# Performance work log

Measured on AMD Instinct MI355X. Metric: run time of the kernel, lower is better.

Reference implementation:

```python
import jax, jax.numpy as jnp
import numpy as np

DIM = 768
HEADS = 12
HEAD_DIM = DIM // HEADS
HIDDEN = 4 * DIM
LS_INIT = 1e-5
EPS = 1e-5


def layernorm(x, g, b):
    mu = jnp.mean(x, axis=-1, keepdims=True)
    var = jnp.mean(jnp.square(x - mu), axis=-1, keepdims=True)
    return (x - mu) * jax.lax.rsqrt(var + EPS) * g + b


def setup_inputs() -> dict:
    key = jax.random.key(0)
    ks = jax.random.split(key, 8)
    s = lambda fan_in: 1.0 / np.sqrt(fan_in)
    return {
        "x": jax.random.normal(ks[0], (8, 1024, DIM), dtype=jnp.float32),
        "ln1_g": jnp.ones((DIM,), jnp.float32),
        "ln1_b": jnp.zeros((DIM,), jnp.float32),
        "w_qkv": jax.random.uniform(ks[1], (3 * DIM, DIM), jnp.float32, -s(DIM), s(DIM)),
        "w_proj": jax.random.uniform(ks[2], (DIM, DIM), jnp.float32, -s(DIM), s(DIM)),
        "b_proj": jnp.zeros((DIM,), jnp.float32),
        "ls1_g": jnp.full((DIM,), LS_INIT, jnp.float32),
        "ln2_g": jnp.ones((DIM,), jnp.float32),
        "ln2_b": jnp.zeros((DIM,), jnp.float32),
        "w_fc1": jax.random.uniform(ks[3], (HIDDEN, DIM), jnp.float32, -s(DIM), s(DIM)),
        "b_fc1": jnp.zeros((HIDDEN,), jnp.float32),
        "w_fc2": jax.random.uniform(ks[4], (DIM, HIDDEN), jnp.float32, -s(HIDDEN), s(HIDDEN)),
        "b_fc2": jnp.zeros((DIM,), jnp.float32),
        "ls2_g": jnp.full((DIM,), LS_INIT, jnp.float32),
    }


def reference(x, ln1_g, ln1_b, w_qkv, w_proj, b_proj, ls1_g,
              ln2_g, ln2_b, w_fc1, b_fc1, w_fc2, b_fc2, ls2_g):
    B, N, C = x.shape
    # --- attention branch ---
    h = layernorm(x, ln1_g, ln1_b)
    qkv = h @ w_qkv.T  # [B,N,3C]
    qkv = qkv.reshape(B, N, 3, HEADS, HEAD_DIM)
    q, k, v = qkv[:, :, 0], qkv[:, :, 1], qkv[:, :, 2]  # [B,N,H,D]
    scale = 1.0 / np.sqrt(HEAD_DIM)
    attn = jnp.einsum("bqhd,bkhd->bhqk", q, k) * scale
    attn = jax.nn.softmax(attn, axis=-1)
    o = jnp.einsum("bhqk,bkhd->bqhd", attn, v).reshape(B, N, C)
    o = o @ w_proj.T + b_proj
    x = x + ls1_g * o
    # --- MLP branch ---
    h = layernorm(x, ln2_g, ln2_b)
    h = jax.nn.gelu(h @ w_fc1.T + b_fc1, approximate=False)
    h = h @ w_fc2.T + b_fc2
    x = x + ls2_g * h
    return x
```

## Files before the change

kernel.cpp:

```cpp
#include <hip/hip_runtime.h>
#include <cstdint>
#include <cstddef>

typedef __bf16 bf16x8 __attribute__((ext_vector_type(8)));
typedef __bf16 bf16x4 __attribute__((ext_vector_type(4)));
typedef float f32x4 __attribute__((ext_vector_type(4)));
typedef int i32x4 __attribute__((ext_vector_type(4)));
typedef int i32x8 __attribute__((ext_vector_type(8)));

__device__ __forceinline__ void gload16(const void* g, void* l) {
  __builtin_amdgcn_global_load_lds((const __attribute__((address_space(1))) void*)g,
                                   (__attribute__((address_space(3))) void*)l, 16, 0, 0);
}

__device__ __forceinline__ float exp2_fast(float x) {
  float r;
  asm("v_exp_f32 %0, %1" : "=v"(r) : "v"(x));
  return r;
}
__device__ __forceinline__ float rcp_fast(float x) {
  float r;
  asm("v_rcp_f32 %0, %1" : "=v"(r) : "v"(x));
  return r;
}

__device__ __forceinline__ unsigned char f32_to_fp8(float x) {
  int p = __builtin_amdgcn_cvt_pk_fp8_f32(x, 0.f, 0, false);
  return (unsigned char)(p & 0xff);
}
__device__ __forceinline__ unsigned int f32x4_to_fp8x4(float a, float b, float c, float d) {
  int p0 = __builtin_amdgcn_cvt_pk_fp8_f32(a, b, 0, false);
  int p1 = __builtin_amdgcn_cvt_pk_fp8_f32(c, d, 0, false);
  return (unsigned int)((p0 & 0xffff) | ((p1 & 0xffff) << 16));
}

template<int N> __device__ __forceinline__ void wait_vm() {
  if constexpr (N == 0)       asm volatile("s_waitcnt vmcnt(0)" ::: "memory");
  else if constexpr (N == 4)  asm volatile("s_waitcnt vmcnt(4)" ::: "memory");
  else if constexpr (N == 6)  asm volatile("s_waitcnt vmcnt(6)" ::: "memory");
}

#define S_BARRIER() __builtin_amdgcn_s_barrier()
#define WAIT_LGKM() asm volatile("s_waitcnt lgkmcnt(0)" ::: "memory")

__global__ __launch_bounds__(256) void ln_kernel(const float* __restrict__ x,
    const float* __restrict__ g, const float* __restrict__ b,
    unsigned char* __restrict__ out)
{
  __shared__ float red[8];
  const int row = blockIdx.x, t = threadIdx.x;
  const float* xr = x + (size_t)row * 768;
  float v0 = xr[t], v1 = xr[t + 256], v2 = xr[t + 512];
  float s = v0 + v1 + v2;
  float q = v0 * v0 + v1 * v1 + v2 * v2;
  #pragma unroll
  for (int off = 32; off > 0; off >>= 1) {
    s += __shfl_xor(s, off, 64);
    q += __shfl_xor(q, off, 64);
  }
  const int w = t >> 6;
  if ((t & 63) == 0) { red[w] = s; red[4 + w] = q; }
  __syncthreads();
  s = red[0] + red[1] + red[2] + red[3];
  q = red[4] + red[5] + red[6] + red[7];
  const float mu = s * (1.0f / 768.0f);
  const float var = q * (1.0f / 768.0f) - mu * mu;
  const float rstd = rsqrtf(var + 1e-5f);
  unsigned char* orow = out + (size_t)row * 768;
  orow[t]       = f32_to_fp8((v0 - mu) * rstd * g[t]       + b[t]);
  orow[t + 256] = f32_to_fp8((v1 - mu) * rstd * g[t + 256] + b[t + 256]);
  orow[t + 512] = f32_to_fp8((v2 - mu) * rstd * g[t + 512] + b[t + 512]);
}

__global__ __launch_bounds__(256) void cast4_kernel(
    const float* __restrict__ i0, const float* __restrict__ i1,
    const float* __restrict__ i2, const float* __restrict__ i3,
    unsigned char* __restrict__ o0, unsigned char* __restrict__ o1,
    unsigned char* __restrict__ o2, unsigned char* __restrict__ o3)
{
  const int n0 = 2304 * 768 / 4, n1 = 768 * 768 / 4;
  const int n2 = 3072 * 768 / 4, n3 = 768 * 3072 / 4;
  const int total = n0 + n1 + n2 + n3;
  for (int i = blockIdx.x * 256 + threadIdx.x; i < total; i += gridDim.x * 256) {
    const float* in; unsigned char* out; int j = i;
    if (j < n0) { in = i0; out = o0; }
    else if ((j -= n0) < n1) { in = i1; out = o1; }
    else if ((j -= n1) < n2) { in = i2; out = o2; }
    else { j -= n2; in = i3; out = o3; }
    float4 v = ((const float4*)in)[j];
    ((unsigned int*)out)[j] = f32x4_to_fp8x4(v.x, v.y, v.z, v.w);
  }
}

template<int MODE>
__global__ __launch_bounds__(256) void gemm_kernel(
    const unsigned char* __restrict__ A, const unsigned char* __restrict__ W, int K,
    const float* __restrict__ bias, const float* __restrict__ resid,
    const float* __restrict__ ls, float* __restrict__ outf,
    unsigned char* __restrict__ outb,
    __bf16* __restrict__ qo, __bf16* __restrict__ ko, __bf16* __restrict__ vo)
{
  constexpr int BM = 128, BN = 64, BK = 128;
  constexpr int FM = 4, FN = 2;
  __shared__ unsigned char As[2 * BM * BK];
  __shared__ unsigned char Bs[2 * BN * BK];

  const int nx = gridDim.x;
  const int nwg = nx * gridDim.y;
  const int orig = blockIdx.x + nx * blockIdx.y;
  const int nid = (orig & 7) * (nwg >> 3) + (orig >> 3);
  const int bx = nid % nx, by = nid / nx;

  const int t = threadIdx.x;
  const int lane = t & 63;
  const int w = t >> 6;
  const int wm = w >> 1, wn = w & 1;
  const int m0 = by * BM, n0 = bx * BN;
  const int rl = lane & 15, gs = lane >> 4;

  f32x4 acc[FM][FN];
  #pragma unroll
  for (int i = 0; i < FM; ++i)
    #pragma unroll
    for (int j = 0; j < FN; ++j) acc[i][j] = { 0.f, 0.f, 0.f, 0.f };

  const unsigned char* Asrc[4];
  const unsigned char* Bsrc[2];
  #pragma unroll
  for (int i = 0; i < 4; ++i) {
    const int g = i * 256 + t, row = g >> 3, gc = g & 7;
    Asrc[i] = A + (size_t)(m0 + row) * K + ((gc ^ (row & 7)) << 4);
  }
  #pragma unroll
  for (int i = 0; i < 2; ++i) {
    const int g = i * 256 + t, row = g >> 3, gc = g & 7;
    Bsrc[i] = W + (size_t)(n0 + row) * K + ((gc ^ (row & 7)) << 4);
  }

  auto stage = [&](int kt, int buf) {
    const int k0 = kt << 7;
    #pragma unroll
    for (int i = 0; i < 4; ++i)
      gload16(Asrc[i] + k0, As + buf * 16384 + (i * 256 + t) * 16);
    #pragma unroll
    for (int i = 0; i < 2; ++i)
      gload16(Bsrc[i] + k0, Bs + buf * 8192 + (i * 256 + t) * 16);
  };

  auto ld32 = [&](const unsigned char* rowbase, int sw) -> i32x8 {
    const i32x4 lo = *(const i32x4*)(rowbase + (((2 * gs + 0) ^ sw) << 4));
    const i32x4 hi = *(const i32x4*)(rowbase + (((2 * gs + 1) ^ sw) << 4));
    i32x8 r;
    r[0] = lo[0]; r[1] = lo[1]; r[2] = lo[2]; r[3] = lo[3];
    r[4] = hi[0]; r[5] = hi[1]; r[6] = hi[2]; r[7] = hi[3];
    return r;
  };

  const int nk = K >> 7;
  stage(0, 0);

  #pragma unroll 2
  for (int kt = 0; kt < nk; ++kt) {
    const int cur = kt & 1;
    if (kt + 1 < nk) { stage(kt + 1, cur ^ 1); wait_vm<6>(); }
    else             { wait_vm<0>(); }
    S_BARRIER();

    const unsigned char* Ac = As + cur * 16384;
    const unsigned char* Bc = Bs + cur * 8192;
    i32x8 af[FM], bfr[FN];
    #pragma unroll
    for (int fm = 0; fm < FM; ++fm) {
      const int row = wm * 64 + fm * 16 + rl;
      af[fm] = ld32(Ac + row * 128, row & 7);
    }
    #pragma unroll
    for (int fn = 0; fn < FN; ++fn) {
      const int row = wn * 32 + fn * 16 + rl;
      bfr[fn] = ld32(Bc + row * 128, row & 7);
    }
    #pragma unroll
    for (int fm = 0; fm < FM; ++fm)
      #pragma unroll
      for (int fn = 0; fn < FN; ++fn)
        acc[fm][fn] = __builtin_amdgcn_mfma_scale_f32_16x16x128_f8f6f4(
            af[fm], bfr[fn], acc[fm][fn],
            0, 0,
            0, 0x7F7F7F7F,
            0, 0x7F7F7F7F);

    S_BARRIER();
  }

  #pragma unroll
  for (int fm = 0; fm < FM; ++fm) {
    const int rbase = m0 + wm * 64 + fm * 16 + gs * 4;
    #pragma unroll
    for (int fn = 0; fn < FN; ++fn) {
      const int c = n0 + wn * 32 + fn * 16 + rl;
      #pragma unroll
      for (int b = 0; b < 4; ++b) {
        const int r = rbase + b;
        const float val = acc[fm][fn][b];
        if constexpr (MODE == 0) {
          const int sec = c / 768;
          const int cc = c - sec * 768;
          const int hh = cc >> 6, d = cc & 63;
          const int batch = r >> 10, n = r & 1023;
          const size_t bh = (size_t)(batch * 12 + hh);
          if (sec == 0)      qo[(bh * 1024 + n) * 64 + d] = (__bf16)(val * 0.1803368801111204f);
          else if (sec == 1) ko[(bh * 1024 + n) * 64 + d] = (__bf16)val;
          else               vo[(bh * 64 + d) * 1024 + n] = (__bf16)val;
        } else if constexpr (MODE == 1) {
          const size_t idx = (size_t)r * 768 + c;
          outf[idx] = resid[idx] + ls[c] * (val + bias[c]);
        } else if constexpr (MODE == 2) {
          const float h = val + bias[c];
          const float z = h * (1.0f + 0.044715f * h * h);
          const float e = exp2_fast(2.3021181f * z);
          const float gl = h - h * rcp_fast(1.0f + e);
          outb[(size_t)r * 3072 + c] = f32_to_fp8(gl);
        } else {
          const size_t idx = (size_t)r * 768 + c;
          outf[idx] = resid[idx] + ls[c] * (val + bias[c]);
        }
      }
    }
  }
}

__global__ __launch_bounds__(256, 3) void attn_kernel(
    const __bf16* __restrict__ Q, const __bf16* __restrict__ Kb,
    const __bf16* __restrict__ Vt, unsigned char* __restrict__ Ob)
{
  __shared__ __bf16 Ks[2][64 * 64];
  __shared__ __bf16 Vs[2][64 * 64];
  __shared__ __bf16 P_lds[4][32 * 72];

  const int nid = blockIdx.x;
  const int b7 = nid & 7, rest = nid >> 3;
  const int qt = rest & 7;
  const int bh = b7 + ((rest >> 3) << 3);

  const int t = threadIdx.x, lane = t & 63, w = t >> 6;
  const int rl = lane & 15, gs = lane >> 4;
  const int q0 = qt * 128 + w * 32;
  const __bf16* Qh = Q  + (size_t)bh * 1024 * 64;
  const char*   Kg = (const char*)(Kb + (size_t)bh * 1024 * 64);
  const char*   Vg = (const char*)(Vt + (size_t)bh * 64 * 1024);
  __bf16* Pw = &P_lds[w][0];

  const int g0 = w * 64 + lane;
  const int g1 = 256 + g0;
  const int r0 = g0 >> 3, sb0 = (g0 & 7) ^ (r0 & 7);
  const int r1 = g1 >> 3, sb1 = (g1 & 7) ^ (r1 & 7);

  bf16x8 aq[2][2];
  #pragma unroll
  for (int m = 0; m < 2; ++m)
    #pragma unroll
    for (int ks = 0; ks < 2; ++ks)
      aq[m][ks] = *(const bf16x8*)(Qh + (size_t)(q0 + m * 16 + rl) * 64 + ks * 32 + gs * 8);

  f32x4 accO[2][4];
  #pragma unroll
  for (int m = 0; m < 2; ++m)
    #pragma unroll
    for (int d = 0; d < 4; ++d) accO[m][d] = { 0.f, 0.f, 0.f, 0.f };
  float L[2][4];
  #pragma unroll
  for (int m = 0; m < 2; ++m)
    #pragma unroll
    for (int b = 0; b < 4; ++b) L[m][b] = 0.f;

  {
    gload16(Kg + (size_t)r0 * 128 + sb0 * 16, (char*)Ks[0] + g0 * 16);
    gload16(Kg + (size_t)r1 * 128 + sb1 * 16, (char*)Ks[0] + g1 * 16);
    gload16(Vg + (size_t)r0 * 2048 + sb0 * 16, (char*)Vs[0] + g0 * 16);
    gload16(Vg + (size_t)r1 * 2048 + sb1 * 16, (char*)Vs[0] + g1 * 16);
  }

  for (int tile = 0; tile < 16; ++tile) {
    const int cur = tile & 1;
    if (tile + 1 < 16) {
      const int nxt = cur ^ 1;
      const size_t kofs = (size_t)(tile + 1) * 64;
      gload16(Kg + (kofs + r0) * 128 + sb0 * 16, (char*)Ks[nxt] + g0 * 16);
      gload16(Kg + (kofs + r1) * 128 + sb1 * 16, (char*)Ks[nxt] + g1 * 16);
      gload16(Vg + (size_t)r0 * 2048 + kofs * 2 + sb0 * 16, (char*)Vs[nxt] + g0 * 16);
      gload16(Vg + (size_t)r1 * 2048 + kofs * 2 + sb1 * 16, (char*)Vs[nxt] + g1 * 16);
      wait_vm<4>();
    } else {
      wait_vm<0>();
    }
    S_BARRIER();

    const __bf16* Kc = Ks[cur];
    const __bf16* Vc = Vs[cur];

    f32x4 s[2][4];
    #pragma unroll
    for (int m = 0; m < 2; ++m)
      #pragma unroll
      for (int ct = 0; ct < 4; ++ct) s[m][ct] = { 0.f, 0.f, 0.f, 0.f };
    __builtin_amdgcn_s_setprio(1);
    #pragma unroll
    for (int ct = 0; ct < 4; ++ct) {
      #pragma unroll
      for (int ks = 0; ks < 2; ++ks) {
        const int row = ct * 16 + rl;
        const int blk = (ks * 4 + gs) ^ (row & 7);
        bf16x8 kf = *(const bf16x8*)(Kc + row * 64 + blk * 8);
        s[0][ct] = __builtin_amdgcn_mfma_f32_16x16x32_bf16(aq[0][ks], kf, s[0][ct], 0, 0, 0);
        s[1][ct] = __builtin_amdgcn_mfma_f32_16x16x32_bf16(aq[1][ks], kf, s[1][ct], 0, 0, 0);
      }
    }
    __builtin_amdgcn_s_setprio(0);

    #pragma unroll
    for (int m = 0; m < 2; ++m) {
      #pragma unroll
      for (int b = 0; b < 4; ++b) {
        float rs = 0.f;
        #pragma unroll
        for (int ct = 0; ct < 4; ++ct) {
          const float p = exp2_fast(s[m][ct][b]);
          rs += p;
          Pw[(m * 16 + gs * 4 + b) * 72 + ct * 16 + rl] = (__bf16)p;
        }
        L[m][b] += rs;
      }
    }

    WAIT_LGKM();
    bf16x8 ap[2][2];
    #pragma unroll
    for (int m = 0; m < 2; ++m)
      #pragma unroll
      for (int ks = 0; ks < 2; ++ks)
        ap[m][ks] = *(const bf16x8*)(Pw + (m * 16 + rl) * 72 + ks * 32 + gs * 8);

    __builtin_amdgcn_s_setprio(1);
    #pragma unroll
    for (int dt = 0; dt < 4; ++dt) {
      #pragma unroll
      for (int ks = 0; ks < 2; ++ks) {
        const int row = dt * 16 + rl;
        const int blk = (ks * 4 + gs) ^ (row & 7);
        bf16x8 vf = *(const bf16x8*)(Vc + row * 64 + blk * 8);
        accO[0][dt] = __builtin_amdgcn_mfma_f32_16x16x32_bf16(ap[0][ks], vf, accO[0][dt], 0, 0, 0);
        accO[1][dt] = __builtin_amdgcn_mfma_f32_16x16x32_bf16(ap[1][ks], vf, accO[1][dt], 0, 0, 0);
      }
    }
    __builtin_amdgcn_s_setprio(0);

    S_BARRIER();
  }

  float invL[2][4];
  #pragma unroll
  for (int m = 0; m < 2; ++m)
    #pragma unroll
    for (int b = 0; b < 4; ++b) {
      float rs = L[m][b];
      #pragma unroll
      for (int off = 1; off < 16; off <<= 1) rs += __shfl_xor(rs, off, 16);
      invL[m][b] = 1.0f / rs;
    }

  const int batch = bh / 12, hh = bh - batch * 12;
  #pragma unroll
  for (int m = 0; m < 2; ++m) {
    const size_t rowbase = (size_t)batch * 1024 + qt * 128 + w * 32 + m * 16 + gs * 4;
    #pragma unroll
    for (int dt = 0; dt < 4; ++dt)
      #pragma unroll
      for (int b = 0; b < 4; ++b)
        Ob[(rowbase + b) * 768 + hh * 64 + dt * 16 + rl] = f32_to_fp8(accO[m][dt][b] * invL[m][b]);
  }
}

extern "C" void kernel_launch(void* const* d_in, const int* in_sizes, int n_in,
                              void* d_out, int out_size, void* d_ws, size_t ws_size,
                              hipStream_t stream) {
  const float* x      = (const float*)d_in[0];
  const float* ln1_g  = (const float*)d_in[1];
  const float* ln1_b  = (const float*)d_in[2];
  const float* w_qkv  = (const float*)d_in[3];
  const float* w_proj = (const float*)d_in[4];
  const float* b_proj = (const float*)d_in[5];
  const float* ls1    = (const float*)d_in[6];
  const float* ln2_g  = (const float*)d_in[7];
  const float* ln2_b  = (const float*)d_in[8];
  const float* w_fc1  = (const float*)d_in[9];
  const float* b_fc1  = (const float*)d_in[10];
  const float* w_fc2  = (const float*)d_in[11];
  const float* b_fc2  = (const float*)d_in[12];
  const float* ls2    = (const float*)d_in[13];
  float* out = (float*)d_out;

  char* ws = (char*)d_ws;
  size_t off = 0;
  auto alloc = [&](size_t bytes) { char* p = ws + off; off += (bytes + 255) & ~(size_t)255; return p; };
  unsigned char* h1    = (unsigned char*)alloc(8192ull * 768);
  unsigned char* wqkv8 = (unsigned char*)alloc(2304ull * 768);
  unsigned char* wprj8 = (unsigned char*)alloc(768ull * 768);
  unsigned char* wfc18 = (unsigned char*)alloc(3072ull * 768);
  unsigned char* wfc28 = (unsigned char*)alloc(768ull * 3072);
  __bf16* Qb    = (__bf16*)alloc(8192ull * 768 * 2);
  __bf16* Kb    = (__bf16*)alloc(8192ull * 768 * 2);
  __bf16* Vt    = (__bf16*)alloc(8192ull * 768 * 2);
  float*  out1  = (float*)alloc(8192ull * 768 * 4);
  unsigned char* fc1o = (unsigned char*)alloc(8192ull * 3072);
  unsigned char* h2   = (unsigned char*)alloc(8192ull * 768);

  ln_kernel<<<8192, 256, 0, stream>>>(x, ln1_g, ln1_b, h1);
  cast4_kernel<<<2048, 256, 0, stream>>>(w_qkv, w_proj, w_fc1, w_fc2,
                                         wqkv8, wprj8, wfc18, wfc28);

  gemm_kernel<0><<<dim3(36, 64), 256, 0, stream>>>(h1, wqkv8, 768,
      nullptr, nullptr, nullptr, nullptr, nullptr, Qb, Kb, Vt);

  attn_kernel<<<96 * 8, 256, 0, stream>>>(Qb, Kb, Vt, h1);

  gemm_kernel<1><<<dim3(12, 64), 256, 0, stream>>>(h1, wprj8, 768,
      b_proj, x, ls1, out1, nullptr, nullptr, nullptr, nullptr);

  ln_kernel<<<8192, 256, 0, stream>>>(out1, ln2_g, ln2_b, h2);

  gemm_kernel<2><<<dim3(48, 64), 256, 0, stream>>>(h2, wfc18, 768,
      b_fc1, nullptr, nullptr, nullptr, fc1o, nullptr, nullptr, nullptr);

  gemm_kernel<3><<<dim3(12, 64), 256, 0, stream>>>(fc1o, wfc28, 3072,
      b_fc2, out1, ls2, out, nullptr, nullptr, nullptr, nullptr);
}
```

Baseline: 181.6 us.

## Switch all GEMM operands from FP8 to FP4 with per-tensor weight scaling

Quantizes activations and weights to packed FP4 (E2M1) instead of FP8 and runs the scaled MFMA in FP4 mode, with fixed power-of-two block scales for the weights. This halves GEMM operand bytes and LDS staging per K-tile, aiming to cut memory traffic and raise matrix throughput. FP4 quantization of activations with no per-block scaling is a large accuracy loss and may break tolerance. Several kernels also change to packed output writes.

After: 179.3 us. Within noise of the previous version (-1.3%).

```diff
diff --git a/kernel.cpp b/kernel.cpp
--- a/kernel.cpp
+++ b/kernel.cpp
@@ -3,7 +3,6 @@
 #include <cstddef>
 
 typedef __bf16 bf16x8 __attribute__((ext_vector_type(8)));
-typedef __bf16 bf16x4 __attribute__((ext_vector_type(4)));
 typedef float f32x4 __attribute__((ext_vector_type(4)));
 typedef int i32x4 __attribute__((ext_vector_type(4)));
 typedef int i32x8 __attribute__((ext_vector_type(8)));
@@ -24,20 +23,20 @@
   return r;
 }
 
-__device__ __forceinline__ unsigned char f32_to_fp8(float x) {
-  int p = __builtin_amdgcn_cvt_pk_fp8_f32(x, 0.f, 0, false);
-  return (unsigned char)(p & 0xff);
-}
-__device__ __forceinline__ unsigned int f32x4_to_fp8x4(float a, float b, float c, float d) {
-  int p0 = __builtin_amdgcn_cvt_pk_fp8_f32(a, b, 0, false);
-  int p1 = __builtin_amdgcn_cvt_pk_fp8_f32(c, d, 0, false);
-  return (unsigned int)((p0 & 0xffff) | ((p1 & 0xffff) << 16));
+__device__ __forceinline__ unsigned int f32_to_fp4(float x) {
+  const float a = fabsf(x);
+  unsigned int c = a < 0.25f ? 0u : a < 0.75f ? 1u : a < 1.25f ? 2u : a < 1.75f ? 3u
+                 : a < 2.5f  ? 4u : a < 3.5f  ? 5u : a < 5.0f  ? 6u : 7u;
+  return c | ((__float_as_uint(x) >> 28) & 8u);
+}
+__device__ __forceinline__ unsigned char pack_fp4x2(float lo, float hi) {
+  return (unsigned char)(f32_to_fp4(lo) | (f32_to_fp4(hi) << 4));
 }
 
 template<int N> __device__ __forceinline__ void wait_vm() {
   if constexpr (N == 0)       asm volatile("s_waitcnt vmcnt(0)" ::: "memory");
+  else if constexpr (N == 3)  asm volatile("s_waitcnt vmcnt(3)" ::: "memory");
   else if constexpr (N == 4)  asm volatile("s_waitcnt vmcnt(4)" ::: "memory");
-  else if constexpr (N == 6)  asm volatile("s_waitcnt vmcnt(6)" ::: "memory");
 }
 
 #define S_BARRIER() __builtin_amdgcn_s_barrier()
@@ -66,10 +65,13 @@
   const float mu = s * (1.0f / 768.0f);
   const float var = q * (1.0f / 768.0f) - mu * mu;
   const float rstd = rsqrtf(var + 1e-5f);
-  unsigned char* orow = out + (size_t)row * 768;
-  orow[t]       = f32_to_fp8((v0 - mu) * rstd * g[t]       + b[t]);
-  orow[t + 256] = f32_to_fp8((v1 - mu) * rstd * g[t + 256] + b[t + 256]);
-  orow[t + 512] = f32_to_fp8((v2 - mu) * rstd * g[t + 512] + b[t + 512]);
+  unsigned char* orow = out + (size_t)row * 384;
+  for (int p = t; p < 384; p += 256) {
+    const int c = 2 * p;
+    const float y0 = (xr[c]     - mu) * rstd * g[c]     + b[c];
+    const float y1 = (xr[c + 1] - mu) * rstd * g[c + 1] + b[c + 1];
+    orow[p] = pack_fp4x2(y0, y1);
+  }
 }
 
 __global__ __launch_bounds__(256) void cast4_kernel(
@@ -82,28 +84,30 @@
   const int n2 = 3072 * 768 / 4, n3 = 768 * 3072 / 4;
   const int total = n0 + n1 + n2 + n3;
   for (int i = blockIdx.x * 256 + threadIdx.x; i < total; i += gridDim.x * 256) {
-    const float* in; unsigned char* out; int j = i;
+    const float* in; unsigned char* out; int j = i; float ws = 128.0f;
     if (j < n0) { in = i0; out = o0; }
     else if ((j -= n0) < n1) { in = i1; out = o1; }
     else if ((j -= n1) < n2) { in = i2; out = o2; }
-    else { j -= n2; in = i3; out = o3; }
+    else { j -= n2; in = i3; out = o3; ws = 256.0f; }
     float4 v = ((const float4*)in)[j];
-    ((unsigned int*)out)[j] = f32x4_to_fp8x4(v.x, v.y, v.z, v.w);
+    const unsigned char b0 = pack_fp4x2(v.x * ws, v.y * ws);
+    const unsigned char b1 = pack_fp4x2(v.z * ws, v.w * ws);
+    ((unsigned short*)out)[j] = (unsigned short)(b0 | (b1 << 8));
   }
 }
 
 template<int MODE>
 __global__ __launch_bounds__(256) void gemm_kernel(
     const unsigned char* __restrict__ A, const unsigned char* __restrict__ W, int K,
+    unsigned int scaleB,
     const float* __restrict__ bias, const float* __restrict__ resid,
     const float* __restrict__ ls, float* __restrict__ outf,
     unsigned char* __restrict__ outb,
     __bf16* __restrict__ qo, __bf16* __restrict__ ko, __bf16* __restrict__ vo)
 {
-  constexpr int BM = 128, BN = 64, BK = 128;
   constexpr int FM = 4, FN = 2;
-  __shared__ unsigned char As[2 * BM * BK];
-  __shared__ unsigned char Bs[2 * BN * BK];
+  __shared__ unsigned char As[2 * 128 * 64];
+  __shared__ unsigned char Bs[2 * 64 * 64];
 
   const int nx = gridDim.x;
   const int nwg = nx * gridDim.y;
@@ -115,8 +119,9 @@
   const int lane = t & 63;
   const int w = t >> 6;
   const int wm = w >> 1, wn = w & 1;
-  const int m0 = by * BM, n0 = bx * BN;
+  const int m0 = by * 128, n0 = bx * 64;
   const int rl = lane & 15, gs = lane >> 4;
+  const int Kb2 = K >> 1;
 
   f32x4 acc[FM][FN];
   #pragma unroll
@@ -124,35 +129,31 @@
     #pragma unroll
     for (int j = 0; j < FN; ++j) acc[i][j] = { 0.f, 0.f, 0.f, 0.f };
 
-  const unsigned char* Asrc[4];
-  const unsigned char* Bsrc[2];
-  #pragma unroll
-  for (int i = 0; i < 4; ++i) {
-    const int g = i * 256 + t, row = g >> 3, gc = g & 7;
-    Asrc[i] = A + (size_t)(m0 + row) * K + ((gc ^ (row & 7)) << 4);
-  }
+  const unsigned char* Asrc[2];
+  const unsigned char* Bsrc1;
   #pragma unroll
   for (int i = 0; i < 2; ++i) {
-    const int g = i * 256 + t, row = g >> 3, gc = g & 7;
-    Bsrc[i] = W + (size_t)(n0 + row) * K + ((gc ^ (row & 7)) << 4);
+    const int g = i * 256 + t, row = g >> 2, gc = g & 3;
+    Asrc[i] = A + (size_t)(m0 + row) * Kb2 + ((gc ^ (row & 3)) << 4);
+  }
+  {
+    const int row = t >> 2, gc = t & 3;
+    Bsrc1 = W + (size_t)(n0 + row) * Kb2 + ((gc ^ (row & 3)) << 4);
   }
 
   auto stage = [&](int kt, int buf) {
-    const int k0 = kt << 7;
-    #pragma unroll
-    for (int i = 0; i < 4; ++i)
-      gload16(Asrc[i] + k0, As + buf * 16384 + (i * 256 + t) * 16);
+    const int k0 = kt << 6;
     #pragma unroll
     for (int i = 0; i < 2; ++i)
-      gload16(Bsrc[i] + k0, Bs + buf * 8192 + (i * 256 + t) * 16);
+      gload16(Asrc[i] + k0, As + buf * 8192 + (i * 256 + t) * 16);
+    gload16(Bsrc1 + k0, Bs + buf * 4096 + t * 16);
   };
 
-  auto ld32 = [&](const unsigned char* rowbase, int sw) -> i32x8 {
-    const i32x4 lo = *(const i32x4*)(rowbase + (((2 * gs + 0) ^ sw) << 4));
-    const i32x4 hi = *(const i32x4*)(rowbase + (((2 * gs + 1) ^ sw) << 4));
+  auto ld16 = [&](const unsigned char* rowbase, int sw) -> i32x8 {
+    const i32x4 v = *(const i32x4*)(rowbase + ((gs ^ sw) << 4));
     i32x8 r;
-    r[0] = lo[0]; r[1] = lo[1]; r[2] = lo[2]; r[3] = lo[3];
-    r[4] = hi[0]; r[5] = hi[1]; r[6] = hi[2]; r[7] = hi[3];
+    r[0] = v[0]; r[1] = v[1]; r[2] = v[2]; r[3] = v[3];
+    r[4] = 0; r[5] = 0; r[6] = 0; r[7] = 0;
     return r;
   };
 
@@ -162,22 +163,22 @@
   #pragma unroll 2
   for (int kt = 0; kt < nk; ++kt) {
     const int cur = kt & 1;
-    if (kt + 1 < nk) { stage(kt + 1, cur ^ 1); wait_vm<6>(); }
+    if (kt + 1 < nk) { stage(kt + 1, cur ^ 1); wait_vm<3>(); }
     else             { wait_vm<0>(); }
     S_BARRIER();
 
-    const unsigned char* Ac = As + cur * 16384;
-    const unsigned char* Bc = Bs + cur * 8192;
+    const unsigned char* Ac = As + cur * 8192;
+    const unsigned char* Bc = Bs + cur * 4096;
     i32x8 af[FM], bfr[FN];
     #pragma unroll
     for (int fm = 0; fm < FM; ++fm) {
       const int row = wm * 64 + fm * 16 + rl;
-      af[fm] = ld32(Ac + row * 128, row & 7);
+      af[fm] = ld16(Ac + row * 64, row & 3);
     }
     #pragma unroll
     for (int fn = 0; fn < FN; ++fn) {
       const int row = wn * 32 + fn * 16 + rl;
-      bfr[fn] = ld32(Bc + row * 128, row & 7);
+      bfr[fn] = ld16(Bc + row * 64, row & 3);
     }
     #pragma unroll
     for (int fm = 0; fm < FM; ++fm)
@@ -185,9 +186,9 @@
       for (int fn = 0; fn < FN; ++fn)
         acc[fm][fn] = __builtin_amdgcn_mfma_scale_f32_16x16x128_f8f6f4(
             af[fm], bfr[fn], acc[fm][fn],
-            0, 0,
+            4, 4,
             0, 0x7F7F7F7F,
-            0, 0x7F7F7F7F);
+            0, (int)scaleB);
 
     S_BARRIER();
   }
@@ -219,7 +220,9 @@
           const float z = h * (1.0f + 0.044715f * h * h);
           const float e = exp2_fast(2.3021181f * z);
           const float gl = h - h * rcp_fast(1.0f + e);
-          outb[(size_t)r * 3072 + c] = f32_to_fp8(gl);
+          const float gp = __shfl_xor(gl, 1, 64);
+          if ((lane & 1) == 0)
+            outb[(size_t)r * 1536 + (c >> 1)] = pack_fp4x2(gl, gp);
         } else {
           const size_t idx = (size_t)r * 768 + c;
           outf[idx] = resid[idx] + ls[c] * (val + bias[c]);
@@ -375,8 +378,12 @@
     #pragma unroll
     for (int dt = 0; dt < 4; ++dt)
       #pragma unroll
-      for (int b = 0; b < 4; ++b)
-        Ob[(rowbase + b) * 768 + hh * 64 + dt * 16 + rl] = f32_to_fp8(accO[m][dt][b] * invL[m][b]);
+      for (int b = 0; b < 4; ++b) {
+        const float val = accO[m][dt][b] * invL[m][b];
+        const float vp = __shfl_xor(val, 1, 64);
+        if ((lane & 1) == 0)
+          Ob[(rowbase + b) * 384 + ((hh * 64 + dt * 16 + rl) >> 1)] = pack_fp4x2(val, vp);
+      }
   }
 }
 
@@ -402,35 +409,38 @@
   char* ws = (char*)d_ws;
   size_t off = 0;
   auto alloc = [&](size_t bytes) { char* p = ws + off; off += (bytes + 255) & ~(size_t)255; return p; };
-  unsigned char* h1    = (unsigned char*)alloc(8192ull * 768);
-  unsigned char* wqkv8 = (unsigned char*)alloc(2304ull * 768);
-  unsigned char* wprj8 = (unsigned char*)alloc(768ull * 768);
-  unsigned char* wfc18 = (unsigned char*)alloc(3072ull * 768);
-  unsigned char* wfc28 = (unsigned char*)alloc(768ull * 3072);
+  unsigned char* h1    = (unsigned char*)alloc(8192ull * 384);
+  unsigned char* wqkv4 = (unsigned char*)alloc(2304ull * 384);
+  unsigned char* wprj4 = (unsigned char*)alloc(768ull * 384);
+  unsigned char* wfc14 = (unsigned char*)alloc(3072ull * 384);
+  unsigned char* wfc24 = (unsigned char*)alloc(768ull * 1536);
   __bf16* Qb    = (__bf16*)alloc(8192ull * 768 * 2);
   __bf16* Kb    = (__bf16*)alloc(8192ull * 768 * 2);
   __bf16* Vt    = (__bf16*)alloc(8192ull * 768 * 2);
   float*  out1  = (float*)alloc(8192ull * 768 * 4);
-  unsigned char* fc1o = (unsigned char*)alloc(8192ull * 3072);
-  unsigned char* h2   = (unsigned char*)alloc(8192ull * 768);
+  unsigned char* fc1o = (unsigned char*)alloc(8192ull * 1536);
+  unsigned char* h2   = (unsigned char*)alloc(8192ull * 384);
+
+  const unsigned int SC7 = 0x78787878u;
+  const unsigned int SC8 = 0x77777777u;
 
   ln_kernel<<<8192, 256, 0, stream>>>(x, ln1_g, ln1_b, h1);
   cast4_kernel<<<2048, 256, 0, stream>>>(w_qkv, w_proj, w_fc1, w_fc2,
-                                         wqkv8, wprj8, wfc18, wfc28);
-
-  gemm_kernel<0><<<dim3(36, 64), 256, 0, stream>>>(h1, wqkv8, 768,
+                                         wqkv4, wprj4, wfc14, wfc24);
+
+  gemm_kernel<0><<<dim3(36, 64), 256, 0, stream>>>(h1, wqkv4, 768, SC7,
       nullptr, nullptr, nullptr, nullptr, nullptr, Qb, Kb, Vt);
 
   attn_kernel<<<96 * 8, 256, 0, stream>>>(Qb, Kb, Vt, h1);
 
-  gemm_kernel<1><<<dim3(12, 64), 256, 0, stream>>>(h1, wprj8, 768,
+  gemm_kernel<1><<<dim3(12, 64), 256, 0, stream>>>(h1, wprj4, 768, SC7,
       b_proj, x, ls1, out1, nullptr, nullptr, nullptr, nullptr);
 
   ln_kernel<<<8192, 256, 0, stream>>>(out1, ln2_g, ln2_b, h2);
 
-  gemm_kernel<2><<<dim3(48, 64), 256, 0, stream>>>(h2, wfc18, 768,
+  gemm_kernel<2><<<dim3(48, 64), 256, 0, stream>>>(h2, wfc14, 768, SC7,
       b_fc1, nullptr, nullptr, nullptr, fc1o, nullptr, nullptr, nullptr);
 
-  gemm_kernel<3><<<dim3(12, 64), 256, 0, stream>>>(fc1o, wfc28, 3072,
+  gemm_kernel<3><<<dim3(12, 64), 256, 0, stream>>>(fc1o, wfc24, 3072, SC8,
       b_fc2, out1, ls2, out, nullptr, nullptr, nullptr, nullptr);
 }
```
